# Kernel optimization log

Hardware: AMD Instinct MI355X
Metric: run time of the kernel (lower is better)

## Reference

```python
import jax, jax.numpy as jnp
import numpy as np

N_NODES = 100000
N_EDGES = 1600000
NODE_DIM = 32
MSG_DIM = 32
COORD_DIM = 3
FF_HALF = 4  # FourierLayer(1, 8) -> coeff [1, 4]


def silu(x):
    return x * jax.nn.sigmoid(x)


def setup_inputs() -> dict:
    key = jax.random.key(0)
    ks = jax.random.split(key, 16)
    s = lambda fan_in: 1.0 / np.sqrt(fan_in)
    edge_in = 2 * NODE_DIM + 2 * FF_HALF  # 72
    node_in = MSG_DIM + NODE_DIM          # 64
    return {
        "coord": jax.random.normal(ks[0], (N_NODES, COORD_DIM), jnp.float32),
        "node_feat": jax.random.normal(ks[1], (N_NODES, NODE_DIM), jnp.float32),
        "edge_index": jax.random.randint(ks[2], (2, N_EDGES), 0, N_NODES, jnp.int64 if jax.config.jax_enable_x64 else jnp.int32),
        "ff_coeff": jax.random.normal(ks[3], (1, FF_HALF), jnp.float32),  # sigma=1.0
        "ew1": jax.random.uniform(ks[4], (edge_in, MSG_DIM), jnp.float32, -s(edge_in), s(edge_in)),
        "eb1": jax.random.uniform(ks[5], (MSG_DIM,), jnp.float32, -s(edge_in), s(edge_in)),
        "ew2": jax.random.uniform(ks[6], (MSG_DIM, MSG_DIM), jnp.float32, -s(MSG_DIM), s(MSG_DIM)),
        "eb2": jax.random.uniform(ks[7], (MSG_DIM,), jnp.float32, -s(MSG_DIM), s(MSG_DIM)),
        "cw1": jax.random.uniform(ks[8], (MSG_DIM, MSG_DIM), jnp.float32, -s(MSG_DIM), s(MSG_DIM)),
        "cb1": jax.random.uniform(ks[9], (MSG_DIM,), jnp.float32, -s(MSG_DIM), s(MSG_DIM)),
        "cw2": jax.random.uniform(ks[10], (MSG_DIM, 1), jnp.float32, -s(MSG_DIM), s(MSG_DIM)),  # bias-free last coord layer
        "nw1": jax.random.uniform(ks[11], (node_in, MSG_DIM), jnp.float32, -s(node_in), s(node_in)),
        "nb1": jax.random.uniform(ks[12], (MSG_DIM,), jnp.float32, -s(node_in), s(node_in)),
        "nw2": jax.random.uniform(ks[13], (MSG_DIM, NODE_DIM), jnp.float32, -s(MSG_DIM), s(MSG_DIM)),
        "nb2": jax.random.uniform(ks[14], (NODE_DIM,), jnp.float32, -s(MSG_DIM), s(MSG_DIM)),
    }


def reference(coord, node_feat, edge_index, ff_coeff, ew1, eb1, ew2, eb2,
              cw1, cb1, cw2, nw1, nb1, nw2, nb2):
    n = coord.shape[0]
    idx_i, idx_j = edge_index[0], edge_index[1]
    # coord2radial (sparse, normalize=False)
    coord_diff = coord[idx_i] - coord[idx_j]                 # [E, 3]
    radial = jnp.sum(coord_diff * coord_diff, axis=1, keepdims=True)  # [E, 1]
    # Fourier radial features (ffr=True): ff1(radial) -> [E, 8]
    x_proj = (2.0 * jnp.pi) * (radial @ ff_coeff)            # [E, 4]
    ff = jnp.concatenate([jnp.cos(x_proj), jnp.sin(x_proj)], axis=-1)  # [E, 8]
    # edge MLP
    edge_in = jnp.concatenate([node_feat[idx_i], node_feat[idx_j], ff], axis=1)  # [E, 72]
    m = silu(edge_in @ ew1 + eb1)
    m = silu(m @ ew2 + eb2)                                  # [E, M]
    # coord model: per-edge scalar weight on coord_diff, mean-aggregated to nodes
    w = silu(m @ cw1 + cb1) @ cw2                            # [E, 1]
    trans = coord_diff * w                                   # [E, 3]
    agg_c = jax.ops.segment_sum(trans, idx_i, num_segments=n)
    counts = jax.ops.segment_sum(jnp.ones((trans.shape[0],), trans.dtype), idx_i, num_segments=n)
    coord_out = coord + agg_c / jnp.clip(counts, 1.0)[:, None]
    # node model: sum-aggregated messages, residual
    agg_h = jax.ops.segment_sum(m, idx_i, num_segments=n)    # [N, M]
    h = silu(jnp.concatenate([node_feat, agg_h], axis=1) @ nw1 + nb1)
    h = h @ nw2 + nb2
    node_out = node_feat + h                                 # is_residual=True
    return node_out, coord_out
```

## Files before the change

### kernel.cpp

```cpp
#include <hip/hip_runtime.h>
#include <math.h>

#ifndef M_PIf
#define M_PIf 3.14159265358979323846f
#endif

__device__ __forceinline__ float silu_f(float x) {
    return x / (1.0f + __expf(-x));
}

#define EW1_OFF 0
#define EB1_OFF 2304
#define EW2_OFF 2336
#define EB2_OFF 3360
#define CW1_OFF 3392
#define CB1_OFF 4416
#define CW2_OFF 4448
#define EDGE_W_TOTAL 4480

__device__ __forceinline__ void stage_edge_weights(
    float* sw,
    const float* __restrict__ ew1, const float* __restrict__ eb1,
    const float* __restrict__ ew2, const float* __restrict__ eb2,
    const float* __restrict__ cw1, const float* __restrict__ cb1,
    const float* __restrict__ cw2)
{
    for (int t = threadIdx.x; t < 2304; t += 256) sw[EW1_OFF + t] = ew1[t];
    for (int t = threadIdx.x; t < 32;   t += 256) sw[EB1_OFF + t] = eb1[t];
    for (int t = threadIdx.x; t < 1024; t += 256) sw[EW2_OFF + t] = ew2[t];
    for (int t = threadIdx.x; t < 32;   t += 256) sw[EB2_OFF + t] = eb2[t];
    for (int t = threadIdx.x; t < 1024; t += 256) sw[CW1_OFF + t] = cw1[t];
    for (int t = threadIdx.x; t < 32;   t += 256) sw[CB1_OFF + t] = cb1[t];
    for (int t = threadIdx.x; t < 32;   t += 256) sw[CW2_OFF + t] = cw2[t];
}

__device__ __forceinline__ void edge_core(
    const float* __restrict__ sw,
    const float* __restrict__ coord,
    const float* __restrict__ node_feat,
    const float* __restrict__ ff_coeff,
    int i, int j,
    float* __restrict__ m,
    float& cdx, float& cdy, float& cdz, float& w)
{
    const float cix = coord[3*(size_t)i+0], ciy = coord[3*(size_t)i+1], ciz = coord[3*(size_t)i+2];
    const float cjx = coord[3*(size_t)j+0], cjy = coord[3*(size_t)j+1], cjz = coord[3*(size_t)j+2];
    cdx = cix - cjx; cdy = ciy - cjy; cdz = ciz - cjz;
    const float radial = cdx*cdx + cdy*cdy + cdz*cdz;

    float ff[8];
    #pragma unroll
    for (int k = 0; k < 4; ++k) {
        float xp = (2.0f * M_PIf) * radial * ff_coeff[k];
        float s, c;
        sincosf(xp, &s, &c);
        ff[k]     = c;
        ff[4 + k] = s;
    }

    float acc[32];
    #pragma unroll
    for (int o = 0; o < 32; ++o) acc[o] = sw[EB1_OFF + o];

    {
        const float4* nfi4 = reinterpret_cast<const float4*>(node_feat + (size_t)i * 32);
        for (int q = 0; q < 8; ++q) {
            float4 v = nfi4[q];
            float xs[4] = {v.x, v.y, v.z, v.w};
            const float* wr = &sw[EW1_OFF + q * 4 * 32];
            #pragma unroll
            for (int kk = 0; kk < 4; ++kk) {
                #pragma unroll
                for (int o = 0; o < 32; ++o)
                    acc[o] = fmaf(xs[kk], wr[kk*32 + o], acc[o]);
            }
        }
        const float4* nfj4 = reinterpret_cast<const float4*>(node_feat + (size_t)j * 32);
        for (int q = 0; q < 8; ++q) {
            float4 v = nfj4[q];
            float xs[4] = {v.x, v.y, v.z, v.w};
            const float* wr = &sw[EW1_OFF + (32 + q * 4) * 32];
            #pragma unroll
            for (int kk = 0; kk < 4; ++kk) {
                #pragma unroll
                for (int o = 0; o < 32; ++o)
                    acc[o] = fmaf(xs[kk], wr[kk*32 + o], acc[o]);
            }
        }
        #pragma unroll
        for (int k = 0; k < 8; ++k) {
            const float* wr = &sw[EW1_OFF + (64 + k) * 32];
            #pragma unroll
            for (int o = 0; o < 32; ++o)
                acc[o] = fmaf(ff[k], wr[o], acc[o]);
        }
    }

    float m1[32];
    #pragma unroll
    for (int o = 0; o < 32; ++o) m1[o] = silu_f(acc[o]);

    #pragma unroll
    for (int o = 0; o < 32; ++o) m[o] = sw[EB2_OFF + o];
    #pragma unroll
    for (int h = 0; h < 32; ++h) {
        #pragma unroll
        for (int o = 0; o < 32; ++o)
            m[o] = fmaf(m1[h], sw[EW2_OFF + h*32 + o], m[o]);
    }
    #pragma unroll
    for (int o = 0; o < 32; ++o) m[o] = silu_f(m[o]);

    float c1[32];
    #pragma unroll
    for (int o = 0; o < 32; ++o) c1[o] = sw[CB1_OFF + o];
    #pragma unroll
    for (int h = 0; h < 32; ++h) {
        #pragma unroll
        for (int o = 0; o < 32; ++o)
            c1[o] = fmaf(m[h], sw[CW1_OFF + h*32 + o], c1[o]);
    }
    w = 0.0f;
    #pragma unroll
    for (int o = 0; o < 32; ++o) w += silu_f(c1[o]) * sw[CW2_OFF + o];
}


__global__ __launch_bounds__(256) void egc_edge_csr(
    const float* __restrict__ coord,
    const float* __restrict__ node_feat,
    const int*   __restrict__ edge_index,
    const float* __restrict__ ff_coeff,
    const float* __restrict__ ew1, const float* __restrict__ eb1,
    const float* __restrict__ ew2, const float* __restrict__ eb2,
    const float* __restrict__ cw1, const float* __restrict__ cb1,
    const float* __restrict__ cw2,
    float* __restrict__ m_buf,
    float* __restrict__ trans4,
    int*   __restrict__ counts,
    int E)
{
    __shared__ float sw[EDGE_W_TOTAL];
    stage_edge_weights(sw, ew1, eb1, ew2, eb2, cw1, cb1, cw2);
    __syncthreads();

    const int e = blockIdx.x * 256 + threadIdx.x;
    if (e >= E) return;

    const int i = edge_index[e];
    const int j = edge_index[E + e];

    float m[32], cdx, cdy, cdz, w;
    edge_core(sw, coord, node_feat, ff_coeff, i, j, m, cdx, cdy, cdz, w);

    float4* mb = reinterpret_cast<float4*>(m_buf + (size_t)e * 32);
    #pragma unroll
    for (int q = 0; q < 8; ++q) {
        float4 v;
        v.x = m[4*q+0]; v.y = m[4*q+1]; v.z = m[4*q+2]; v.w = m[4*q+3];
        mb[q] = v;
    }
    float4 t; t.x = cdx * w; t.y = cdy * w; t.z = cdz * w; t.w = 0.0f;
    *reinterpret_cast<float4*>(trans4 + (size_t)e * 4) = t;

    atomicAdd(&counts[i], 1);
}

__global__ __launch_bounds__(1024) void egc_scan(
    const int* __restrict__ counts, int* __restrict__ row_start, int N)
{
    __shared__ int wsum[16];
    __shared__ int carry_s;
    const int tid = threadIdx.x;
    const int lane = tid & 63, wid = tid >> 6;
    if (tid == 0) carry_s = 0;
    __syncthreads();
    for (int base = 0; base < N; base += 1024) {
        const int idx = base + tid;
        const int x = (idx < N) ? counts[idx] : 0;
        int incl = x;
        #pragma unroll
        for (int off = 1; off < 64; off <<= 1) {
            int v = __shfl_up(incl, off, 64);
            if (lane >= off) incl += v;
        }
        if (lane == 63) wsum[wid] = incl;
        __syncthreads();
        if (wid == 0) {
            int v = (lane < 16) ? wsum[lane] : 0;
            int s = v;
            #pragma unroll
            for (int off = 1; off < 16; off <<= 1) {
                int t = __shfl_up(s, off, 64);
                if (lane >= off) s += t;
            }
            if (lane < 16) wsum[lane] = s - v;
        }
        __syncthreads();
        const int carry = carry_s;
        if (idx < N) row_start[idx] = carry + wsum[wid] + incl - x;
        __syncthreads();
        if (tid == 1023) carry_s = carry + wsum[15] + incl;
        __syncthreads();
    }
    if (tid == 0) row_start[N] = carry_s;
}

__global__ __launch_bounds__(256) void egc_scatter(
    const int* __restrict__ edge_index,
    const int* __restrict__ row_start,
    int* __restrict__ cursor,
    int* __restrict__ edge_order,
    int E)
{
    const int e = blockIdx.x * 256 + threadIdx.x;
    if (e >= E) return;
    const int i = edge_index[e];
    const int pos = atomicAdd(&cursor[i], 1);
    edge_order[row_start[i] + pos] = e;
}

#define NW1_OFF 0
#define NB1_OFF 2048
#define NW2_OFF 2080
#define NB2_OFF 3104
#define NODE_W_TOTAL 3136

__global__ __launch_bounds__(256) void egc_node_csr(
    const float* __restrict__ coord,
    const float* __restrict__ node_feat,
    const float* __restrict__ m_buf,
    const float* __restrict__ trans4,
    const int*   __restrict__ row_start,
    const int*   __restrict__ edge_order,
    const float* __restrict__ nw1, const float* __restrict__ nb1,
    const float* __restrict__ nw2, const float* __restrict__ nb2,
    float* __restrict__ out_node,
    float* __restrict__ out_coord,
    int N)
{
    __shared__ float sw[NODE_W_TOTAL];
    for (int t = threadIdx.x; t < 2048; t += 256) sw[NW1_OFF + t] = nw1[t];
    for (int t = threadIdx.x; t < 32;   t += 256) sw[NB1_OFF + t] = nb1[t];
    for (int t = threadIdx.x; t < 1024; t += 256) sw[NW2_OFF + t] = nw2[t];
    for (int t = threadIdx.x; t < 32;   t += 256) sw[NB2_OFF + t] = nb2[t];
    __syncthreads();

    const int n = blockIdx.x * 256 + threadIdx.x;
    if (n >= N) return;

    const int rs = row_start[n];
    const int re = row_start[n + 1];

    float agg[32];
    #pragma unroll
    for (int o = 0; o < 32; ++o) agg[o] = 0.0f;
    float acx = 0.0f, acy = 0.0f, acz = 0.0f;

    for (int k = rs; k < re; ++k) {
        const int e = edge_order[k];
        const float4* mb = reinterpret_cast<const float4*>(m_buf + (size_t)e * 32);
        #pragma unroll
        for (int q = 0; q < 8; ++q) {
            float4 v = mb[q];
            agg[4*q+0] += v.x; agg[4*q+1] += v.y; agg[4*q+2] += v.z; agg[4*q+3] += v.w;
        }
        float4 t = *reinterpret_cast<const float4*>(trans4 + (size_t)e * 4);
        acx += t.x; acy += t.y; acz += t.z;
    }

    float nf[32];
    {
        const float4* nf4 = reinterpret_cast<const float4*>(node_feat + (size_t)n * 32);
        #pragma unroll
        for (int q = 0; q < 8; ++q) {
            float4 v = nf4[q];
            nf[4*q+0] = v.x; nf[4*q+1] = v.y; nf[4*q+2] = v.z; nf[4*q+3] = v.w;
        }
    }

    float acc[32];
    #pragma unroll
    for (int o = 0; o < 32; ++o) acc[o] = sw[NB1_OFF + o];
    #pragma unroll
    for (int k = 0; k < 32; ++k) {
        #pragma unroll
        for (int o = 0; o < 32; ++o)
            acc[o] = fmaf(nf[k], sw[NW1_OFF + k*32 + o], acc[o]);
    }
    #pragma unroll
    for (int k = 0; k < 32; ++k) {
        #pragma unroll
        for (int o = 0; o < 32; ++o)
            acc[o] = fmaf(agg[k], sw[NW1_OFF + (32+k)*32 + o], acc[o]);
    }
    float h1[32];
    #pragma unroll
    for (int o = 0; o < 32; ++o) h1[o] = silu_f(acc[o]);

    float h2[32];
    #pragma unroll
    for (int o = 0; o < 32; ++o) h2[o] = sw[NB2_OFF + o];
    #pragma unroll
    for (int k = 0; k < 32; ++k) {
        #pragma unroll
        for (int o = 0; o < 32; ++o)
            h2[o] = fmaf(h1[k], sw[NW2_OFF + k*32 + o], h2[o]);
    }

    {
        float4* on4 = reinterpret_cast<float4*>(out_node + (size_t)n * 32);
        #pragma unroll
        for (int q = 0; q < 8; ++q) {
            float4 v;
            v.x = nf[4*q+0] + h2[4*q+0];
            v.y = nf[4*q+1] + h2[4*q+1];
            v.z = nf[4*q+2] + h2[4*q+2];
            v.w = nf[4*q+3] + h2[4*q+3];
            on4[q] = v;
        }
    }

    const float deg = (float)(re - rs);
    const float inv = 1.0f / fmaxf(deg, 1.0f);
    out_coord[(size_t)n*3 + 0] = coord[(size_t)n*3 + 0] + acx * inv;
    out_coord[(size_t)n*3 + 1] = coord[(size_t)n*3 + 1] + acy * inv;
    out_coord[(size_t)n*3 + 2] = coord[(size_t)n*3 + 2] + acz * inv;
}


__global__ __launch_bounds__(256) void egc_edge_fb(
    const float* __restrict__ coord,
    const float* __restrict__ node_feat,
    const int*   __restrict__ edge_index,
    const float* __restrict__ ff_coeff,
    const float* __restrict__ ew1, const float* __restrict__ eb1,
    const float* __restrict__ ew2, const float* __restrict__ eb2,
    const float* __restrict__ cw1, const float* __restrict__ cb1,
    const float* __restrict__ cw2,
    float* __restrict__ agg_h, float* __restrict__ agg_c, float* __restrict__ counts,
    int E)
{
    __shared__ float sw[EDGE_W_TOTAL];
    stage_edge_weights(sw, ew1, eb1, ew2, eb2, cw1, cb1, cw2);
    __syncthreads();

    const int e = blockIdx.x * 256 + threadIdx.x;
    if (e >= E) return;
    const int i = edge_index[e];
    const int j = edge_index[E + e];

    float m[32], cdx, cdy, cdz, w;
    edge_core(sw, coord, node_feat, ff_coeff, i, j, m, cdx, cdy, cdz, w);

    float* dst = agg_h + (size_t)i * 32;
    #pragma unroll
    for (int o = 0; o < 32; ++o) atomicAdd(&dst[o], m[o]);
    atomicAdd(&agg_c[(size_t)i*3 + 0], cdx * w);
    atomicAdd(&agg_c[(size_t)i*3 + 1], cdy * w);
    atomicAdd(&agg_c[(size_t)i*3 + 2], cdz * w);
    atomicAdd(&counts[i], 1.0f);
}

__global__ __launch_bounds__(256) void egc_node_fb(
    const float* __restrict__ coord,
    const float* __restrict__ node_feat,
    const float* __restrict__ agg_h,
    const float* __restrict__ agg_c,
    const float* __restrict__ counts,
    const float* __restrict__ nw1, const float* __restrict__ nb1,
    const float* __restrict__ nw2, const float* __restrict__ nb2,
    float* __restrict__ out_node, float* __restrict__ out_coord, int N)
{
    __shared__ float sw[NODE_W_TOTAL];
    for (int t = threadIdx.x; t < 2048; t += 256) sw[NW1_OFF + t] = nw1[t];
    for (int t = threadIdx.x; t < 32;   t += 256) sw[NB1_OFF + t] = nb1[t];
    for (int t = threadIdx.x; t < 1024; t += 256) sw[NW2_OFF + t] = nw2[t];
    for (int t = threadIdx.x; t < 32;   t += 256) sw[NB2_OFF + t] = nb2[t];
    __syncthreads();

    const int n = blockIdx.x * 256 + threadIdx.x;
    if (n >= N) return;

    float nf[32];
    {
        const float4* nf4 = reinterpret_cast<const float4*>(node_feat + (size_t)n * 32);
        #pragma unroll
        for (int q = 0; q < 8; ++q) {
            float4 v = nf4[q];
            nf[4*q+0] = v.x; nf[4*q+1] = v.y; nf[4*q+2] = v.z; nf[4*q+3] = v.w;
        }
    }
    float acc[32];
    #pragma unroll
    for (int o = 0; o < 32; ++o) acc[o] = sw[NB1_OFF + o];
    #pragma unroll
    for (int k = 0; k < 32; ++k) {
        #pragma unroll
        for (int o = 0; o < 32; ++o)
            acc[o] = fmaf(nf[k], sw[NW1_OFF + k*32 + o], acc[o]);
    }
    {
        const float4* ah4 = reinterpret_cast<const float4*>(agg_h + (size_t)n * 32);
        #pragma unroll
        for (int q = 0; q < 8; ++q) {
            float4 v = ah4[q];
            float xs[4] = {v.x, v.y, v.z, v.w};
            const float* wr = &sw[NW1_OFF + (32 + q * 4) * 32];
            #pragma unroll
            for (int kk = 0; kk < 4; ++kk) {
                #pragma unroll
                for (int o = 0; o < 32; ++o)
                    acc[o] = fmaf(xs[kk], wr[kk*32 + o], acc[o]);
            }
        }
    }
    float h1[32];
    #pragma unroll
    for (int o = 0; o < 32; ++o) h1[o] = silu_f(acc[o]);
    float h2[32];
    #pragma unroll
    for (int o = 0; o < 32; ++o) h2[o] = sw[NB2_OFF + o];
    #pragma unroll
    for (int k = 0; k < 32; ++k) {
        #pragma unroll
        for (int o = 0; o < 32; ++o)
            h2[o] = fmaf(h1[k], sw[NW2_OFF + k*32 + o], h2[o]);
    }
    {
        float4* on4 = reinterpret_cast<float4*>(out_node + (size_t)n * 32);
        #pragma unroll
        for (int q = 0; q < 8; ++q) {
            float4 v;
            v.x = nf[4*q+0] + h2[4*q+0];
            v.y = nf[4*q+1] + h2[4*q+1];
            v.z = nf[4*q+2] + h2[4*q+2];
            v.w = nf[4*q+3] + h2[4*q+3];
            on4[q] = v;
        }
    }
    const float cnt = fmaxf(counts[n], 1.0f);
    const float inv = 1.0f / cnt;
    out_coord[(size_t)n*3 + 0] = coord[(size_t)n*3 + 0] + agg_c[(size_t)n*3 + 0] * inv;
    out_coord[(size_t)n*3 + 1] = coord[(size_t)n*3 + 1] + agg_c[(size_t)n*3 + 1] * inv;
    out_coord[(size_t)n*3 + 2] = coord[(size_t)n*3 + 2] + agg_c[(size_t)n*3 + 2] * inv;
}


extern "C" void kernel_launch(void* const* d_in, const int* in_sizes, int n_in,
                              void* d_out, int out_size, void* d_ws, size_t ws_size,
                              hipStream_t stream) {
    const float* coord     = (const float*)d_in[0];
    const float* node_feat = (const float*)d_in[1];
    const int*   edge_index= (const int*)  d_in[2];
    const float* ff_coeff  = (const float*)d_in[3];
    const float* ew1 = (const float*)d_in[4];
    const float* eb1 = (const float*)d_in[5];
    const float* ew2 = (const float*)d_in[6];
    const float* eb2 = (const float*)d_in[7];
    const float* cw1 = (const float*)d_in[8];
    const float* cb1 = (const float*)d_in[9];
    const float* cw2 = (const float*)d_in[10];
    const float* nw1 = (const float*)d_in[11];
    const float* nb1 = (const float*)d_in[12];
    const float* nw2 = (const float*)d_in[13];
    const float* nb2 = (const float*)d_in[14];

    const int N = in_sizes[0] / 3;
    const int E = in_sizes[2] / 2;

    float* out_node  = (float*)d_out;
    float* out_coord = out_node + (size_t)N * 32;

    const size_t m_off      = 0;
    const size_t t_off      = m_off + (size_t)E * 32;
    const size_t eo_off     = t_off + (size_t)E * 4;
    const size_t cnt_off    = eo_off + (size_t)E;
    const size_t cur_off    = cnt_off + (size_t)N;
    const size_t rs_off     = cur_off + (size_t)N;
    const size_t need_bytes = (rs_off + (size_t)N + 1) * 4 + 256;

    if (ws_size >= need_bytes) {
        float* m_buf      = (float*)d_ws + m_off;
        float* trans4     = (float*)d_ws + t_off;
        int*   edge_order = (int*)d_ws + eo_off;
        int*   counts     = (int*)d_ws + cnt_off;
        int*   cursor     = (int*)d_ws + cur_off;
        int*   row_start  = (int*)d_ws + rs_off;

        hipMemsetAsync(counts, 0, (size_t)2 * N * sizeof(int), stream);

        egc_edge_csr<<<(E + 255) / 256, 256, 0, stream>>>(
            coord, node_feat, edge_index, ff_coeff,
            ew1, eb1, ew2, eb2, cw1, cb1, cw2,
            m_buf, trans4, counts, E);

        egc_scan<<<1, 1024, 0, stream>>>(counts, row_start, N);

        egc_scatter<<<(E + 255) / 256, 256, 0, stream>>>(
            edge_index, row_start, cursor, edge_order, E);

        egc_node_csr<<<(N + 255) / 256, 256, 0, stream>>>(
            coord, node_feat, m_buf, trans4, row_start, edge_order,
            nw1, nb1, nw2, nb2, out_node, out_coord, N);
    } else {
        float* agg_h  = (float*)d_ws;
        float* agg_c  = agg_h + (size_t)N * 32;
        float* counts = agg_c + (size_t)N * 3;
        hipMemsetAsync(d_ws, 0, (size_t)N * 36 * sizeof(float), stream);

        egc_edge_fb<<<(E + 255) / 256, 256, 0, stream>>>(
            coord, node_feat, edge_index, ff_coeff,
            ew1, eb1, ew2, eb2, cw1, cb1, cw2,
            agg_h, agg_c, counts, E);

        egc_node_fb<<<(N + 255) / 256, 256, 0, stream>>>(
            coord, node_feat, agg_h, agg_c, counts,
            nw1, nb1, nw2, nb2, out_node, out_coord, N);
    }
}
```

Measured before the change: 767.8 us.

## Build CSR first and write edge messages directly into sorted slots

Edge count histogram and scan now run before the edge MLP, and the edge kernel claims a slot per destination node via an atomic cursor so messages are written in CSR order. The node kernel then reads its messages contiguously instead of through an edge_order indirection, and the scatter kernel and edge_order array are removed. Separately, all weight staging into shared memory is dropped in favour of direct global/constant-cache reads of the uniform weights. This adds an extra pass over idx_i and relies on scalar-cache loads for the weights, which may be slower than LDS.

```diff
diff --git a/kernel.cpp b/kernel.cpp
--- a/kernel.cpp
+++ b/kernel.cpp
@@ -9,36 +9,14 @@
     return x / (1.0f + __expf(-x));
 }
 
-#define EW1_OFF 0
-#define EB1_OFF 2304
-#define EW2_OFF 2336
-#define EB2_OFF 3360
-#define CW1_OFF 3392
-#define CB1_OFF 4416
-#define CW2_OFF 4448
-#define EDGE_W_TOTAL 4480
-
-__device__ __forceinline__ void stage_edge_weights(
-    float* sw,
+__device__ __forceinline__ void edge_core(
+    const float* __restrict__ coord,
+    const float* __restrict__ node_feat,
+    const float* __restrict__ ff_coeff,
     const float* __restrict__ ew1, const float* __restrict__ eb1,
     const float* __restrict__ ew2, const float* __restrict__ eb2,
     const float* __restrict__ cw1, const float* __restrict__ cb1,
-    const float* __restrict__ cw2)
-{
-    for (int t = threadIdx.x; t < 2304; t += 256) sw[EW1_OFF + t] = ew1[t];
-    for (int t = threadIdx.x; t < 32;   t += 256) sw[EB1_OFF + t] = eb1[t];
-    for (int t = threadIdx.x; t < 1024; t += 256) sw[EW2_OFF + t] = ew2[t];
-    for (int t = threadIdx.x; t < 32;   t += 256) sw[EB2_OFF + t] = eb2[t];
-    for (int t = threadIdx.x; t < 1024; t += 256) sw[CW1_OFF + t] = cw1[t];
-    for (int t = threadIdx.x; t < 32;   t += 256) sw[CB1_OFF + t] = cb1[t];
-    for (int t = threadIdx.x; t < 32;   t += 256) sw[CW2_OFF + t] = cw2[t];
-}
-
-__device__ __forceinline__ void edge_core(
-    const float* __restrict__ sw,
-    const float* __restrict__ coord,
-    const float* __restrict__ node_feat,
-    const float* __restrict__ ff_coeff,
+    const float* __restrict__ cw2,
     int i, int j,
     float* __restrict__ m,
     float& cdx, float& cdy, float& cdz, float& w)
@@ -60,14 +38,14 @@
 
     float acc[32];
     #pragma unroll
-    for (int o = 0; o < 32; ++o) acc[o] = sw[EB1_OFF + o];
+    for (int o = 0; o < 32; ++o) acc[o] = eb1[o];
 
     {
         const float4* nfi4 = reinterpret_cast<const float4*>(node_feat + (size_t)i * 32);
         for (int q = 0; q < 8; ++q) {
             float4 v = nfi4[q];
             float xs[4] = {v.x, v.y, v.z, v.w};
-            const float* wr = &sw[EW1_OFF + q * 4 * 32];
+            const float* wr = ew1 + q * 4 * 32;
             #pragma unroll
             for (int kk = 0; kk < 4; ++kk) {
                 #pragma unroll
@@ -79,7 +57,7 @@
         for (int q = 0; q < 8; ++q) {
             float4 v = nfj4[q];
             float xs[4] = {v.x, v.y, v.z, v.w};
-            const float* wr = &sw[EW1_OFF + (32 + q * 4) * 32];
+            const float* wr = ew1 + (32 + q * 4) * 32;
             #pragma unroll
             for (int kk = 0; kk < 4; ++kk) {
                 #pragma unroll
@@ -89,7 +67,7 @@
         }
         #pragma unroll
         for (int k = 0; k < 8; ++k) {
-            const float* wr = &sw[EW1_OFF + (64 + k) * 32];
+            const float* wr = ew1 + (64 + k) * 32;
             #pragma unroll
             for (int o = 0; o < 32; ++o)
                 acc[o] = fmaf(ff[k], wr[o], acc[o]);
@@ -101,73 +79,41 @@
     for (int o = 0; o < 32; ++o) m1[o] = silu_f(acc[o]);
 
     #pragma unroll
-    for (int o = 0; o < 32; ++o) m[o] = sw[EB2_OFF + o];
+    for (int o = 0; o < 32; ++o) m[o] = eb2[o];
     #pragma unroll
     for (int h = 0; h < 32; ++h) {
         #pragma unroll
         for (int o = 0; o < 32; ++o)
-            m[o] = fmaf(m1[h], sw[EW2_OFF + h*32 + o], m[o]);
+            m[o] = fmaf(m1[h], ew2[h*32 + o], m[o]);
     }
     #pragma unroll
     for (int o = 0; o < 32; ++o) m[o] = silu_f(m[o]);
 
     float c1[32];
     #pragma unroll
-    for (int o = 0; o < 32; ++o) c1[o] = sw[CB1_OFF + o];
+    for (int o = 0; o < 32; ++o) c1[o] = cb1[o];
     #pragma unroll
     for (int h = 0; h < 32; ++h) {
         #pragma unroll
         for (int o = 0; o < 32; ++o)
-            c1[o] = fmaf(m[h], sw[CW1_OFF + h*32 + o], c1[o]);
+            c1[o] = fmaf(m[h], cw1[h*32 + o], c1[o]);
     }
     w = 0.0f;
     #pragma unroll
-    for (int o = 0; o < 32; ++o) w += silu_f(c1[o]) * sw[CW2_OFF + o];
-}
-
-
-__global__ __launch_bounds__(256) void egc_edge_csr(
-    const float* __restrict__ coord,
-    const float* __restrict__ node_feat,
-    const int*   __restrict__ edge_index,
-    const float* __restrict__ ff_coeff,
-    const float* __restrict__ ew1, const float* __restrict__ eb1,
-    const float* __restrict__ ew2, const float* __restrict__ eb2,
-    const float* __restrict__ cw1, const float* __restrict__ cb1,
-    const float* __restrict__ cw2,
-    float* __restrict__ m_buf,
-    float* __restrict__ trans4,
-    int*   __restrict__ counts,
-    int E)
-{
-    __shared__ float sw[EDGE_W_TOTAL];
-    stage_edge_weights(sw, ew1, eb1, ew2, eb2, cw1, cb1, cw2);
-    __syncthreads();
-
+    for (int o = 0; o < 32; ++o) w += silu_f(c1[o]) * cw2[o];
+}
+
+
+__global__ __launch_bounds__(256) void egc_hist(
+    const int* __restrict__ idx_i, int* __restrict__ counts, int E)
+{
     const int e = blockIdx.x * 256 + threadIdx.x;
-    if (e >= E) return;
-
-    const int i = edge_index[e];
-    const int j = edge_index[E + e];
-
-    float m[32], cdx, cdy, cdz, w;
-    edge_core(sw, coord, node_feat, ff_coeff, i, j, m, cdx, cdy, cdz, w);
-
-    float4* mb = reinterpret_cast<float4*>(m_buf + (size_t)e * 32);
-    #pragma unroll
-    for (int q = 0; q < 8; ++q) {
-        float4 v;
-        v.x = m[4*q+0]; v.y = m[4*q+1]; v.z = m[4*q+2]; v.w = m[4*q+3];
-        mb[q] = v;
-    }
-    float4 t; t.x = cdx * w; t.y = cdy * w; t.z = cdz * w; t.w = 0.0f;
-    *reinterpret_cast<float4*>(trans4 + (size_t)e * 4) = t;
-
-    atomicAdd(&counts[i], 1);
+    if (e < E) atomicAdd(&counts[idx_i[e]], 1);
 }
 
 __global__ __launch_bounds__(1024) void egc_scan(
-    const int* __restrict__ counts, int* __restrict__ row_start, int N)
+    const int* __restrict__ counts, int* __restrict__ row_start,
+    int* __restrict__ cursor, int N)
 {
     __shared__ int wsum[16];
     __shared__ int carry_s;
@@ -198,7 +144,11 @@
         }
         __syncthreads();
         const int carry = carry_s;
-        if (idx < N) row_start[idx] = carry + wsum[wid] + incl - x;
+        if (idx < N) {
+            const int v = carry + wsum[wid] + incl - x;
+            row_start[idx] = v;
+            cursor[idx]    = v;
+        }
         __syncthreads();
         if (tid == 1023) carry_s = carry + wsum[15] + incl;
         __syncthreads();
@@ -206,46 +156,54 @@
     if (tid == 0) row_start[N] = carry_s;
 }
 
-__global__ __launch_bounds__(256) void egc_scatter(
-    const int* __restrict__ edge_index,
-    const int* __restrict__ row_start,
-    int* __restrict__ cursor,
-    int* __restrict__ edge_order,
+__global__ __launch_bounds__(256) void egc_edge_direct(
+    const float* __restrict__ coord,
+    const float* __restrict__ node_feat,
+    const int*   __restrict__ edge_index,
+    const float* __restrict__ ff_coeff,
+    const float* __restrict__ ew1, const float* __restrict__ eb1,
+    const float* __restrict__ ew2, const float* __restrict__ eb2,
+    const float* __restrict__ cw1, const float* __restrict__ cb1,
+    const float* __restrict__ cw2,
+    int*   __restrict__ cursor,
+    float* __restrict__ m_buf,
+    float* __restrict__ trans4,
     int E)
 {
     const int e = blockIdx.x * 256 + threadIdx.x;
     if (e >= E) return;
+
     const int i = edge_index[e];
-    const int pos = atomicAdd(&cursor[i], 1);
-    edge_order[row_start[i] + pos] = e;
-}
-
-#define NW1_OFF 0
-#define NB1_OFF 2048
-#define NW2_OFF 2080
-#define NB2_OFF 3104
-#define NODE_W_TOTAL 3136
-
-__global__ __launch_bounds__(256) void egc_node_csr(
+    const int j = edge_index[E + e];
+    const int slot = atomicAdd(&cursor[i], 1);
+
+    float m[32], cdx, cdy, cdz, w;
+    edge_core(coord, node_feat, ff_coeff, ew1, eb1, ew2, eb2, cw1, cb1, cw2,
+              i, j, m, cdx, cdy, cdz, w);
+
+    float4* mb = reinterpret_cast<float4*>(m_buf + (size_t)slot * 32);
+    #pragma unroll
+    for (int q = 0; q < 8; ++q) {
+        float4 v;
+        v.x = m[4*q+0]; v.y = m[4*q+1]; v.z = m[4*q+2]; v.w = m[4*q+3];
+        mb[q] = v;
+    }
+    float4 t; t.x = cdx * w; t.y = cdy * w; t.z = cdz * w; t.w = 0.0f;
+    *reinterpret_cast<float4*>(trans4 + (size_t)slot * 4) = t;
+}
+
+__global__ __launch_bounds__(256) void egc_node_direct(
     const float* __restrict__ coord,
     const float* __restrict__ node_feat,
     const float* __restrict__ m_buf,
     const float* __restrict__ trans4,
     const int*   __restrict__ row_start,
-    const int*   __restrict__ edge_order,
     const float* __restrict__ nw1, const float* __restrict__ nb1,
     const float* __restrict__ nw2, const float* __restrict__ nb2,
     float* __restrict__ out_node,
     float* __restrict__ out_coord,
     int N)
 {
-    __shared__ float sw[NODE_W_TOTAL];
-    for (int t = threadIdx.x; t < 2048; t += 256) sw[NW1_OFF + t] = nw1[t];
-    for (int t = threadIdx.x; t < 32;   t += 256) sw[NB1_OFF + t] = nb1[t];
-    for (int t = threadIdx.x; t < 1024; t += 256) sw[NW2_OFF + t] = nw2[t];
-    for (int t = threadIdx.x; t < 32;   t += 256) sw[NB2_OFF + t] = nb2[t];
-    __syncthreads();
-
     const int n = blockIdx.x * 256 + threadIdx.x;
     if (n >= N) return;
 
@@ -258,14 +216,13 @@
     float acx = 0.0f, acy = 0.0f, acz = 0.0f;
 
     for (int k = rs; k < re; ++k) {
-        const int e = edge_order[k];
-        const float4* mb = reinterpret_cast<const float4*>(m_buf + (size_t)e * 32);
+        const float4* mb = reinterpret_cast<const float4*>(m_buf + (size_t)k * 32);
         #pragma unroll
         for (int q = 0; q < 8; ++q) {
             float4 v = mb[q];
             agg[4*q+0] += v.x; agg[4*q+1] += v.y; agg[4*q+2] += v.z; agg[4*q+3] += v.w;
         }
-        float4 t = *reinterpret_cast<const float4*>(trans4 + (size_t)e * 4);
+        float4 t = *reinterpret_cast<const float4*>(trans4 + (size_t)k * 4);
         acx += t.x; acy += t.y; acz += t.z;
     }
 
@@ -281,18 +238,18 @@
 
     float acc[32];
     #pragma unroll
-    for (int o = 0; o < 32; ++o) acc[o] = sw[NB1_OFF + o];
+    for (int o = 0; o < 32; ++o) acc[o] = nb1[o];
     #pragma unroll
     for (int k = 0; k < 32; ++k) {
         #pragma unroll
         for (int o = 0; o < 32; ++o)
-            acc[o] = fmaf(nf[k], sw[NW1_OFF + k*32 + o], acc[o]);
+            acc[o] = fmaf(nf[k], nw1[k*32 + o], acc[o]);
     }
     #pragma unroll
     for (int k = 0; k < 32; ++k) {
         #pragma unroll
         for (int o = 0; o < 32; ++o)
-            acc[o] = fmaf(agg[k], sw[NW1_OFF + (32+k)*32 + o], acc[o]);
+            acc[o] = fmaf(agg[k], nw1[(32+k)*32 + o], acc[o]);
     }
     float h1[32];
     #pragma unroll
@@ -300,12 +257,12 @@
 
     float h2[32];
     #pragma unroll
-    for (int o = 0; o < 32; ++o) h2[o] = sw[NB2_OFF + o];
+    for (int o = 0; o < 32; ++o) h2[o] = nb2[o];
     #pragma unroll
     for (int k = 0; k < 32; ++k) {
         #pragma unroll
         for (int o = 0; o < 32; ++o)
-            h2[o] = fmaf(h1[k], sw[NW2_OFF + k*32 + o], h2[o]);
+            h2[o] = fmaf(h1[k], nw2[k*32 + o], h2[o]);
     }
 
     {
@@ -341,17 +298,14 @@
     float* __restrict__ agg_h, float* __restrict__ agg_c, float* __restrict__ counts,
     int E)
 {
-    __shared__ float sw[EDGE_W_TOTAL];
-    stage_edge_weights(sw, ew1, eb1, ew2, eb2, cw1, cb1, cw2);
-    __syncthreads();
-
     const int e = blockIdx.x * 256 + threadIdx.x;
     if (e >= E) return;
     const int i = edge_index[e];
     const int j = edge_index[E + e];
 
     float m[32], cdx, cdy, cdz, w;
-    edge_core(sw, coord, node_feat, ff_coeff, i, j, m, cdx, cdy, cdz, w);
+    edge_core(coord, node_feat, ff_coeff, ew1, eb1, ew2, eb2, cw1, cb1, cw2,
+              i, j, m, cdx, cdy, cdz, w);
 
     float* dst = agg_h + (size_t)i * 32;
     #pragma unroll
@@ -372,13 +326,6 @@
     const float* __restrict__ nw2, const float* __restrict__ nb2,
     float* __restrict__ out_node, float* __restrict__ out_coord, int N)
 {
-    __shared__ float sw[NODE_W_TOTAL];
-    for (int t = threadIdx.x; t < 2048; t += 256) sw[NW1_OFF + t] = nw1[t];
-    for (int t = threadIdx.x; t < 32;   t += 256) sw[NB1_OFF + t] = nb1[t];
-    for (int t = threadIdx.x; t < 1024; t += 256) sw[NW2_OFF + t] = nw2[t];
-    for (int t = threadIdx.x; t < 32;   t += 256) sw[NB2_OFF + t] = nb2[t];
-    __syncthreads();
-
     const int n = blockIdx.x * 256 + threadIdx.x;
     if (n >= N) return;
 
@@ -393,12 +340,12 @@
     }
     float acc[32];
     #pragma unroll
-    for (int o = 0; o < 32; ++o) acc[o] = sw[NB1_OFF + o];
+    for (int o = 0; o < 32; ++o) acc[o] = nb1[o];
     #pragma unroll
     for (int k = 0; k < 32; ++k) {
         #pragma unroll
         for (int o = 0; o < 32; ++o)
-            acc[o] = fmaf(nf[k], sw[NW1_OFF + k*32 + o], acc[o]);
+            acc[o] = fmaf(nf[k], nw1[k*32 + o], acc[o]);
     }
     {
         const float4* ah4 = reinterpret_cast<const float4*>(agg_h + (size_t)n * 32);
@@ -406,7 +353,7 @@
         for (int q = 0; q < 8; ++q) {
             float4 v = ah4[q];
             float xs[4] = {v.x, v.y, v.z, v.w};
-            const float* wr = &sw[NW1_OFF + (32 + q * 4) * 32];
+            const float* wr = nw1 + (32 + q * 4) * 32;
             #pragma unroll
             for (int kk = 0; kk < 4; ++kk) {
                 #pragma unroll
@@ -420,12 +367,12 @@
     for (int o = 0; o < 32; ++o) h1[o] = silu_f(acc[o]);
     float h2[32];
     #pragma unroll
-    for (int o = 0; o < 32; ++o) h2[o] = sw[NB2_OFF + o];
+    for (int o = 0; o < 32; ++o) h2[o] = nb2[o];
     #pragma unroll
     for (int k = 0; k < 32; ++k) {
         #pragma unroll
         for (int o = 0; o < 32; ++o)
-            h2[o] = fmaf(h1[k], sw[NW2_OFF + k*32 + o], h2[o]);
+            h2[o] = fmaf(h1[k], nw2[k*32 + o], h2[o]);
     }
     {
         float4* on4 = reinterpret_cast<float4*>(out_node + (size_t)n * 32);
@@ -472,36 +419,33 @@
     float* out_node  = (float*)d_out;
     float* out_coord = out_node + (size_t)N * 32;
 
-    const size_t m_off      = 0;
-    const size_t t_off      = m_off + (size_t)E * 32;
-    const size_t eo_off     = t_off + (size_t)E * 4;
-    const size_t cnt_off    = eo_off + (size_t)E;
-    const size_t cur_off    = cnt_off + (size_t)N;
-    const size_t rs_off     = cur_off + (size_t)N;
+    const size_t m_off   = 0;
+    const size_t t_off   = m_off + (size_t)E * 32;
+    const size_t cnt_off = t_off + (size_t)E * 4;
+    const size_t cur_off = cnt_off + (size_t)N;
+    const size_t rs_off  = cur_off + (size_t)N;
     const size_t need_bytes = (rs_off + (size_t)N + 1) * 4 + 256;
 
     if (ws_size >= need_bytes) {
-        float* m_buf      = (float*)d_ws + m_off;
-        float* trans4     = (float*)d_ws + t_off;
-        int*   edge_order = (int*)d_ws + eo_off;
-        int*   counts     = (int*)d_ws + cnt_off;
-        int*   cursor     = (int*)d_ws + cur_off;
-        int*   row_start  = (int*)d_ws + rs_off;
-
-        hipMemsetAsync(counts, 0, (size_t)2 * N * sizeof(int), stream);
-
-        egc_edge_csr<<<(E + 255) / 256, 256, 0, stream>>>(
+        float* m_buf     = (float*)d_ws + m_off;
+        float* trans4    = (float*)d_ws + t_off;
+        int*   counts    = (int*)d_ws + cnt_off;
+        int*   cursor    = (int*)d_ws + cur_off;
+        int*   row_start = (int*)d_ws + rs_off;
+
+        hipMemsetAsync(counts, 0, (size_t)N * sizeof(int), stream);
+
+        egc_hist<<<(E + 255) / 256, 256, 0, stream>>>(edge_index, counts, E);
+
+        egc_scan<<<1, 1024, 0, stream>>>(counts, row_start, cursor, N);
+
+        egc_edge_direct<<<(E + 255) / 256, 256, 0, stream>>>(
             coord, node_feat, edge_index, ff_coeff,
             ew1, eb1, ew2, eb2, cw1, cb1, cw2,
-            m_buf, trans4, counts, E);
-
-        egc_scan<<<1, 1024, 0, stream>>>(counts, row_start, N);
-
-        egc_scatter<<<(E + 255) / 256, 256, 0, stream>>>(
-            edge_index, row_start, cursor, edge_order, E);
-
-        egc_node_csr<<<(N + 255) / 256, 256, 0, stream>>>(
-            coord, node_feat, m_buf, trans4, row_start, edge_order,
+            cursor, m_buf, trans4, E);
+
+        egc_node_direct<<<(N + 255) / 256, 256, 0, stream>>>(
+            coord, node_feat, m_buf, trans4, row_start,
             nw1, nb1, nw2, nb2, out_node, out_coord, N);
     } else {
         float* agg_h  = (float*)d_ws;
```

New measurement: 818.9 us. 1.07x slower.
